# Kernel tuning notes

Hardware: AMD Instinct MI355X
Metric: run time of the kernel (lower is better)

Reference implementation:

```python
import jax, jax.numpy as jnp
import numpy as np

B, H, L, D, S = 4, 16, 4096, 64, 128

def setup_inputs() -> dict:
    key = jax.random.key(0)
    k1, k2 = jax.random.split(key)
    x = jax.random.normal(k1, (B, H, L, D), dtype=jnp.float32)
    c = jax.random.normal(k2, (H, S, D), dtype=jnp.float32)
    # codebook rows are unit-normalized at init (matches torch init)
    c = c / jnp.linalg.norm(c, axis=-1, keepdims=True)
    return {"x": x, "c": c}

def reference(x, c):
    # cosine-similarity scores: [B,H,L,S]
    cos_sim = jnp.einsum('bhld,hsd->bhls', x, c)
    delta_index = jnp.argmax(cos_sim, axis=-1)            # [B,H,L]
    delta_onehot = jax.nn.one_hot(delta_index, c.shape[-2], dtype=jnp.float32)  # [B,H,L,S]
    return (delta_onehot, c)
```

## Files before the change

kernel.cpp:

```cpp
#include <hip/hip_runtime.h>
#include <math.h>

constexpr int BB = 4;
constexpr int HH = 16;
constexpr int LL = 4096;
constexpr int DD = 64;
constexpr int SS = 128;
constexpr int BM = 128;

constexpr float TAU = 2e-3f;

typedef __attribute__((ext_vector_type(8))) short bf16x8;
typedef __attribute__((ext_vector_type(4))) float f32x4;

#define MFMA16 __builtin_amdgcn_mfma_f32_16x16x32_bf16

__device__ __forceinline__ unsigned short f2bf(float v) {
    unsigned u = __float_as_uint(v);
    return (unsigned short)((u + 0x7fffu + ((u >> 16) & 1u)) >> 16);
}

__device__ __forceinline__ void split8(const float4 va, const float4 vb,
                                       uint4* hi, uint4* lo) {
    const float v[8] = {va.x, va.y, va.z, va.w, vb.x, vb.y, vb.z, vb.w};
    unsigned hw[4], lw[4];
    #pragma unroll
    for (int p = 0; p < 4; ++p) {
        const unsigned u0 = __float_as_uint(v[2 * p]);
        const unsigned u1 = __float_as_uint(v[2 * p + 1]);
        const unsigned h0 = u0 & 0xffff0000u;
        const unsigned h1 = u1 & 0xffff0000u;
        hw[p] = (u0 >> 16) | h1;
        lw[p] = (unsigned)f2bf(v[2 * p] - __uint_as_float(h0))
              | ((unsigned)f2bf(v[2 * p + 1] - __uint_as_float(h1)) << 16);
    }
    *hi = make_uint4(hw[0], hw[1], hw[2], hw[3]);
    *lo = make_uint4(lw[0], lw[1], lw[2], lw[3]);
}

union FragU { uint4 q; bf16x8 v; };

__global__ __launch_bounds__(256) void convert_c_kernel(
    const float* __restrict__ c, unsigned char* __restrict__ ws,
    float* __restrict__ out_c)
{
    const int sid = blockIdx.x * 256 + threadIdx.x;
    const int h  = sid >> 10;
    const int r  = sid & 1023;
    const int kt = r >> 9;
    const int ct = (r >> 6) & 7;
    const int ln = r & 63;
    const int cc = ct * 16 + (ln & 15);
    const int k0 = kt * 32 + (ln >> 4) * 8;
    const float4* src = (const float4*)(c + ((size_t)h * SS + cc) * DD + k0);
    uint4 hi, lo;
    split8(src[0], src[1], &hi, &lo);
    unsigned char* base =
        ws + (size_t)h * 32768 + (size_t)(((kt << 3) | ct) * 1024 + ln * 16);
    *(uint4*)(base) = hi;
    *(uint4*)(base + 16384) = lo;

    const f32x4* __restrict__ s4 = (const f32x4*)c;
    f32x4* __restrict__ d4 = (f32x4*)out_c;
    __builtin_nontemporal_store(s4[sid], d4 + sid);
    __builtin_nontemporal_store(s4[sid + 16384], d4 + sid + 16384);
}

template <bool USE_WS>
__global__ __launch_bounds__(256, 2) void quantizer_kernel(
    const float* __restrict__ x,
    const float* __restrict__ c,
    const unsigned char* __restrict__ ws,
    float* __restrict__ out,
    float* __restrict__ out_c)
{
    __shared__ int s_res[4][32];
    __shared__ int s_wcnt[4];
    __shared__ int s_wlist[4][32];

    const int tid = threadIdx.x;
    const int wv = tid >> 6;
    const int lane = tid & 63;
    const int ln15 = lane & 15;
    const long long r0 = (long long)blockIdx.x * BM;
    const int h = (int)((r0 >> 12) & (HH - 1));
    const float* __restrict__ chead = c + (size_t)h * SS * DD;
    const unsigned char* __restrict__ wsb =
        USE_WS ? (ws + (size_t)h * 32768) : nullptr;
    const int k0 = (lane >> 4) * 8;

    if (lane == 0) s_wcnt[wv] = 0;

    bf16x8 af[2][2][2];
    #pragma unroll
    for (int rtb = 0; rtb < 2; ++rtb) {
        const float* xr =
            x + (size_t)(r0 + wv * 32 + rtb * 16 + ln15) * DD + k0;
        #pragma unroll
        for (int kt = 0; kt < 2; ++kt) {
            FragU hi, lo;
            split8(*(const float4*)(xr + kt * 32),
                   *(const float4*)(xr + kt * 32 + 4), &hi.q, &lo.q);
            af[rtb][kt][0] = hi.v;
            af[rtb][kt][1] = lo.v;
        }
    }

    float m1[2][4], m2[2][4];
    int   mi_[2][4];
    #pragma unroll
    for (int rtb = 0; rtb < 2; ++rtb)
        #pragma unroll
        for (int r = 0; r < 4; ++r) {
            m1[rtb][r] = -INFINITY; m2[rtb][r] = -INFINITY; mi_[rtb][r] = 0;
        }

    #pragma unroll 1
    for (int ct = 0; ct < 8; ++ct) {
        bf16x8 b10, b11, b20, b21;
        if constexpr (USE_WS) {
            const unsigned char* bp = wsb + (unsigned)(ct * 1024 + lane * 16);
            b10 = *(const bf16x8*)(bp);
            b11 = *(const bf16x8*)(bp + 8192);
            b20 = *(const bf16x8*)(bp + 16384);
            b21 = *(const bf16x8*)(bp + 24576);
        } else {
            const float* cr = chead + (size_t)(ct * 16 + ln15) * DD + k0;
            FragU h0, l0, h1, l1;
            split8(*(const float4*)cr, *(const float4*)(cr + 4),
                   &h0.q, &l0.q);
            split8(*(const float4*)(cr + 32), *(const float4*)(cr + 36),
                   &h1.q, &l1.q);
            b10 = h0.v; b20 = l0.v; b11 = h1.v; b21 = l1.v;
        }
        #pragma unroll
        for (int rtb = 0; rtb < 2; ++rtb) {
            f32x4 a0 = {0.f, 0.f, 0.f, 0.f};
            f32x4 a1 = {0.f, 0.f, 0.f, 0.f};
            a0 = MFMA16(af[rtb][0][1], b10, a0, 0, 0, 0);
            a0 = MFMA16(af[rtb][0][0], b20, a0, 0, 0, 0);
            a0 = MFMA16(af[rtb][0][0], b10, a0, 0, 0, 0);
            a1 = MFMA16(af[rtb][1][1], b11, a1, 0, 0, 0);
            a1 = MFMA16(af[rtb][1][0], b21, a1, 0, 0, 0);
            a1 = MFMA16(af[rtb][1][0], b11, a1, 0, 0, 0);
            #pragma unroll
            for (int r = 0; r < 4; ++r) {
                const float v = a0[r] + a1[r];
                const int col = ct * 16 + ln15;
                m2[rtb][r] = __builtin_amdgcn_fmed3f(m1[rtb][r], v, m2[rtb][r]);
                if (v > m1[rtb][r]) { m1[rtb][r] = v; mi_[rtb][r] = col; }
            }
        }
    }

    #pragma unroll
    for (int rtb = 0; rtb < 2; ++rtb) {
        int rv[4];
        #pragma unroll
        for (int r = 0; r < 4; ++r) {
            float a1 = m1[rtb][r], a2 = m2[rtb][r];
            int ai = mi_[rtb][r];
            #pragma unroll
            for (int off = 1; off <= 8; off <<= 1) {
                const float o1 = __shfl_xor(a1, off);
                const float o2 = __shfl_xor(a2, off);
                const int   oi = __shfl_xor(ai, off);
                const bool take = (o1 > a1) || (o1 == a1 && oi < ai);
                const float n2 = take ? fmaxf(a1, o2) : fmaxf(a2, o1);
                if (take) { a1 = o1; ai = oi; }
                a2 = n2;
            }
            rv[r] = ai;
            if (ln15 == 0 && (a1 - a2) < TAU) {
                const int p = atomicAdd(&s_wcnt[wv], 1);
                s_wlist[wv][p] = rtb * 16 + (lane >> 4) * 4 + r;
            }
        }
        if (ln15 == 0)
            *(int4*)&s_res[wv][rtb * 16 + (lane >> 4) * 4] =
                make_int4(rv[0], rv[1], rv[2], rv[3]);
    }

    const int cnt = s_wcnt[wv];
    for (int f = 0; f < cnt; ++f) {
        const int local = s_wlist[wv][f];
        const float4* __restrict__ xr =
            (const float4*)(x + (size_t)(r0 + wv * 32 + local) * DD);
        const float4* __restrict__ c0 =
            (const float4*)(chead + (size_t)lane * DD);
        const float4* __restrict__ c1 =
            (const float4*)(chead + (size_t)(lane + 64) * DD);
        float s0 = 0.f, s1 = 0.f;
        #pragma unroll
        for (int q = 0; q < 16; ++q) {
            const float4 a = xr[q];
            const float4 b0 = c0[q];
            const float4 b1 = c1[q];
            s0 = fmaf(a.x, b0.x, s0); s0 = fmaf(a.y, b0.y, s0);
            s0 = fmaf(a.z, b0.z, s0); s0 = fmaf(a.w, b0.w, s0);
            s1 = fmaf(a.x, b1.x, s1); s1 = fmaf(a.y, b1.y, s1);
            s1 = fmaf(a.z, b1.z, s1); s1 = fmaf(a.w, b1.w, s1);
        }
        float v = s0; int bi = lane;
        if (s1 > v) { v = s1; bi = lane + 64; }
        #pragma unroll
        for (int off = 1; off < 64; off <<= 1) {
            const float ov = __shfl_xor(v, off);
            const int   oi = __shfl_xor(bi, off);
            if (ov > v || (ov == v && oi < bi)) { v = ov; bi = oi; }
        }
        if (lane == 0) s_res[wv][local] = bi;
    }

    f32x4* __restrict__ op = (f32x4*)(out + (size_t)(r0 + wv * 32) * SS);
    #pragma unroll
    for (int k = 0; k < 16; ++k) {
        const int i = lane + k * 64;
        const int am = s_res[wv][i >> 5];
        const int s0 = (i & 31) * 4;
        f32x4 v = {(s0 + 0 == am) ? 1.f : 0.f,
                   (s0 + 1 == am) ? 1.f : 0.f,
                   (s0 + 2 == am) ? 1.f : 0.f,
                   (s0 + 3 == am) ? 1.f : 0.f};
        __builtin_nontemporal_store(v, op + i);
    }

    if (!USE_WS && blockIdx.x < 128) {
        const float4* __restrict__ src = (const float4*)c;
        float4* __restrict__ dst = (float4*)out_c;
        const int idx = blockIdx.x * 256 + tid;
        dst[idx] = src[idx];
    }
}

extern "C" void kernel_launch(void* const* d_in, const int* in_sizes, int n_in,
                              void* d_out, int out_size, void* d_ws, size_t ws_size,
                              hipStream_t stream) {
    const float* x = (const float*)d_in[0];
    const float* c = (const float*)d_in[1];
    float* out = (float*)d_out;
    float* out_c = out + (size_t)BB * HH * LL * SS;

    const int rows = BB * HH * LL;
    const int blocks = rows / BM;
    const size_t ws_need = (size_t)HH * 32768;

    if (d_ws != nullptr && ws_size >= ws_need) {
        convert_c_kernel<<<64, 256, 0, stream>>>(c, (unsigned char*)d_ws,
                                                 out_c);
        quantizer_kernel<true><<<blocks, 256, 0, stream>>>(
            x, c, (const unsigned char*)d_ws, out, out_c);
    } else {
        quantizer_kernel<false><<<blocks, 256, 0, stream>>>(
            x, c, nullptr, out, out_c);
    }
}
```

Before: 202.7 us.

## Switch to one-wavefront blocks and ballot-based near-tie row mask

Each block now holds a single 64-lane wavefront covering 32 rows instead of four wavefronts covering 128 rows, which quadruples the grid and drops the launch-bounds occupancy hint. The shared-memory atomic tie list is replaced by a ballot-built register bitmask that is walked with count-trailing-zeros to run the exact fp32 recheck. This removes LDS atomics and gives the scheduler finer-grained blocks, at the cost of more blocks and possibly different register allocation and occupancy.

```diff
diff --git a/kernel.cpp b/kernel.cpp
--- a/kernel.cpp
+++ b/kernel.cpp
@@ -6,7 +6,7 @@
 constexpr int LL = 4096;
 constexpr int DD = 64;
 constexpr int SS = 128;
-constexpr int BM = 128;
+constexpr int WR = 32;
 
 constexpr float TAU = 2e-3f;
 
@@ -67,35 +67,28 @@
 }
 
 template <bool USE_WS>
-__global__ __launch_bounds__(256, 2) void quantizer_kernel(
+__global__ __launch_bounds__(64) void quantizer_kernel(
     const float* __restrict__ x,
     const float* __restrict__ c,
     const unsigned char* __restrict__ ws,
     float* __restrict__ out,
     float* __restrict__ out_c)
 {
-    __shared__ int s_res[4][32];
-    __shared__ int s_wcnt[4];
-    __shared__ int s_wlist[4][32];
-
-    const int tid = threadIdx.x;
-    const int wv = tid >> 6;
-    const int lane = tid & 63;
+    __shared__ int s_res[WR];
+
+    const int lane = threadIdx.x;
     const int ln15 = lane & 15;
-    const long long r0 = (long long)blockIdx.x * BM;
+    const long long r0 = (long long)blockIdx.x * WR;
     const int h = (int)((r0 >> 12) & (HH - 1));
     const float* __restrict__ chead = c + (size_t)h * SS * DD;
     const unsigned char* __restrict__ wsb =
         USE_WS ? (ws + (size_t)h * 32768) : nullptr;
     const int k0 = (lane >> 4) * 8;
 
-    if (lane == 0) s_wcnt[wv] = 0;
-
     bf16x8 af[2][2][2];
     #pragma unroll
     for (int rtb = 0; rtb < 2; ++rtb) {
-        const float* xr =
-            x + (size_t)(r0 + wv * 32 + rtb * 16 + ln15) * DD + k0;
+        const float* xr = x + (size_t)(r0 + rtb * 16 + ln15) * DD + k0;
         #pragma unroll
         for (int kt = 0; kt < 2; ++kt) {
             FragU hi, lo;
@@ -153,6 +146,7 @@
         }
     }
 
+    unsigned rowmask = 0;
     #pragma unroll
     for (int rtb = 0; rtb < 2; ++rtb) {
         int rv[4];
@@ -171,21 +165,23 @@
                 a2 = n2;
             }
             rv[r] = ai;
-            if (ln15 == 0 && (a1 - a2) < TAU) {
-                const int p = atomicAdd(&s_wcnt[wv], 1);
-                s_wlist[wv][p] = rtb * 16 + (lane >> 4) * 4 + r;
-            }
+            const unsigned long long b =
+                __ballot((a1 - a2) < TAU) & 0x0001000100010001ULL;
+            rowmask |= ((unsigned)(b) & 1u)         << (rtb * 16 + 0 + r);
+            rowmask |= ((unsigned)(b >> 16) & 1u)   << (rtb * 16 + 4 + r);
+            rowmask |= ((unsigned)(b >> 32) & 1u)   << (rtb * 16 + 8 + r);
+            rowmask |= ((unsigned)(b >> 48) & 1u)   << (rtb * 16 + 12 + r);
         }
         if (ln15 == 0)
-            *(int4*)&s_res[wv][rtb * 16 + (lane >> 4) * 4] =
+            *(int4*)&s_res[rtb * 16 + (lane >> 4) * 4] =
                 make_int4(rv[0], rv[1], rv[2], rv[3]);
     }
 
-    const int cnt = s_wcnt[wv];
-    for (int f = 0; f < cnt; ++f) {
-        const int local = s_wlist[wv][f];
+    while (rowmask) {
+        const int row = __builtin_ctz(rowmask);
+        rowmask &= rowmask - 1;
         const float4* __restrict__ xr =
-            (const float4*)(x + (size_t)(r0 + wv * 32 + local) * DD);
+            (const float4*)(x + (size_t)(r0 + row) * DD);
         const float4* __restrict__ c0 =
             (const float4*)(chead + (size_t)lane * DD);
         const float4* __restrict__ c1 =
@@ -209,14 +205,14 @@
             const int   oi = __shfl_xor(bi, off);
             if (ov > v || (ov == v && oi < bi)) { v = ov; bi = oi; }
         }
-        if (lane == 0) s_res[wv][local] = bi;
-    }
-
-    f32x4* __restrict__ op = (f32x4*)(out + (size_t)(r0 + wv * 32) * SS);
+        if (lane == 0) s_res[row] = bi;
+    }
+
+    f32x4* __restrict__ op = (f32x4*)(out + (size_t)r0 * SS);
     #pragma unroll
     for (int k = 0; k < 16; ++k) {
         const int i = lane + k * 64;
-        const int am = s_res[wv][i >> 5];
+        const int am = s_res[i >> 5];
         const int s0 = (i & 31) * 4;
         f32x4 v = {(s0 + 0 == am) ? 1.f : 0.f,
                    (s0 + 1 == am) ? 1.f : 0.f,
@@ -225,10 +221,10 @@
         __builtin_nontemporal_store(v, op + i);
     }
 
-    if (!USE_WS && blockIdx.x < 128) {
+    if (!USE_WS && blockIdx.x < 512) {
         const float4* __restrict__ src = (const float4*)c;
         float4* __restrict__ dst = (float4*)out_c;
-        const int idx = blockIdx.x * 256 + tid;
+        const int idx = blockIdx.x * 64 + lane;
         dst[idx] = src[idx];
     }
 }
@@ -242,16 +238,16 @@
     float* out_c = out + (size_t)BB * HH * LL * SS;
 
     const int rows = BB * HH * LL;
-    const int blocks = rows / BM;
+    const int blocks = rows / WR;
     const size_t ws_need = (size_t)HH * 32768;
 
     if (d_ws != nullptr && ws_size >= ws_need) {
         convert_c_kernel<<<64, 256, 0, stream>>>(c, (unsigned char*)d_ws,
                                                  out_c);
-        quantizer_kernel<true><<<blocks, 256, 0, stream>>>(
+        quantizer_kernel<true><<<blocks, 64, 0, stream>>>(
             x, c, (const unsigned char*)d_ws, out, out_c);
     } else {
-        quantizer_kernel<false><<<blocks, 256, 0, stream>>>(
+        quantizer_kernel<false><<<blocks, 64, 0, stream>>>(
             x, c, nullptr, out, out_c);
     }
 }
```

New measurement: 203.9 us. Within noise of the previous version (+0.6%).
